# Kernel optimization log

Measured on AMD Instinct MI355X. Metric: run time of the kernel, lower is better.

Reference implementation:

```python
import jax, jax.numpy as jnp
import numpy as np
import math

B, H, S, D = 8, 16, 1024, 64


def setup_inputs() -> dict:
    key = jax.random.key(0)
    kq, kk, kv, kl = jax.random.split(key, 4)
    queries = jax.random.normal(kq, (B * H, S, D), dtype=jnp.float32)
    keys = jax.random.normal(kk, (B * H, S, D), dtype=jnp.float32)
    values = jax.random.normal(kv, (B * H, S, D), dtype=jnp.float32)
    valid_lens = jax.random.randint(kl, (B,), 0, 1024, dtype=jnp.int64)
    return {"queries": queries, "keys": keys, "values": values, "valid_lens": valid_lens}


def reference(queries, keys, values, valid_lens):
    d = queries.shape[-1]
    seq_len = queries.shape[1]
    b = valid_lens.shape[0]
    h = queries.shape[0] // b
    scale = 1.0 / math.sqrt(d)
    # [BH, S, S] scores, faithful to bmm(q, k^T)/sqrt(d)
    scores = jnp.einsum("bqd,bkd->bqk", queries, keys) * scale
    # encode_mask: mask[b, q, k] = (k >= valid_lens[b]) for 1-D valid_lens
    key_mask = jnp.arange(seq_len) >= valid_lens[:, None]  # [B, S]
    scores = scores.reshape(b, h, seq_len, seq_len)
    # masked_fill with 1e-6 (NOT -inf), faithful to the original
    scores = jnp.where(key_mask[:, None, None, :], jnp.float32(1e-6), scores)
    attn = jax.nn.softmax(scores, axis=-1)
    out = jnp.einsum("bhqk,bhkd->bhqd", attn, values.reshape(b, h, seq_len, d))
    return out.reshape(b * h, seq_len, d)
```

## Files before the change

### kernel.cpp

```cpp
#include <hip/hip_runtime.h>
#include <hip/hip_bf16.h>

typedef short short4v __attribute__((ext_vector_type(4)));
typedef short short8v __attribute__((ext_vector_type(8)));
typedef float floatx4 __attribute__((ext_vector_type(4)));

#define SLEN 1024
#define DDIM 64
#define NBH  128
#define PSTR 72

__device__ __forceinline__ unsigned short f2bf(float f) {
  union { float f; unsigned int u; } v; v.f = f;
  unsigned int u = v.u;
  u += 0x7fffu + ((u >> 16) & 1u);
  return (unsigned short)(u >> 16);
}

__device__ __forceinline__ unsigned int pkbf(float a, float b) {
  __hip_bfloat162 h = __float22bfloat162_rn(float2{a, b});
  union { __hip_bfloat162 h; unsigned int u; } c; c.h = h;
  return c.u;
}

__device__ __forceinline__ void ld_lds16(const void* g, void* l) {
  __builtin_amdgcn_global_load_lds(
      (const __attribute__((address_space(1))) void*)g,
      (__attribute__((address_space(3))) void*)l, 16, 0, 0);
}

__global__ __launch_bounds__(256)
void prep_k(const float* __restrict__ Kg, unsigned short* __restrict__ wsK) {
  const int t = blockIdx.x * 256 + threadIdx.x;
  const int tile = t >> 9;
  const int q = t & 511;
  const int r = q >> 3, gr = q & 7;
  const float4 f0 = *(const float4*)(Kg + (size_t)t * 8);
  const float4 f1 = *(const float4*)(Kg + (size_t)t * 8 + 4);
  short8v s;
  s[0]=(short)f2bf(f0.x); s[1]=(short)f2bf(f0.y); s[2]=(short)f2bf(f0.z); s[3]=(short)f2bf(f0.w);
  s[4]=(short)f2bf(f1.x); s[5]=(short)f2bf(f1.y); s[6]=(short)f2bf(f1.z); s[7]=(short)f2bf(f1.w);
  *(short8v*)(wsK + (size_t)tile * 4096 + r * 64 + ((gr ^ (r & 7)) * 8)) = s;
}

__global__ __launch_bounds__(256)
void prep_v(const float* __restrict__ Vg, unsigned short* __restrict__ wsVT,
            float* __restrict__ CS) {
  const int w = threadIdx.x >> 6;
  const int d = threadIdx.x & 63;
  const int tile = blockIdx.x * 4 + w;
  const int bh = tile >> 4, ch = tile & 15;
  const float* src = Vg + ((size_t)(bh * SLEN + ch * 64) * DDIM) + d;
  unsigned short* dst = wsVT + (size_t)tile * 4096 + d * 64;
  float sum = 0.f;
  #pragma unroll
  for (int gg = 0; gg < 8; ++gg) {
    short8v s;
    #pragma unroll
    for (int j = 0; j < 8; ++j) {
      const float x = src[(size_t)(gg * 8 + j) * DDIM];
      sum += x;
      s[j] = (short)f2bf(x);
    }
    *(short8v*)(dst + ((gg ^ (d & 7)) * 8)) = s;
  }
  if (CS) CS[(size_t)tile * 64 + d] = sum;
}

__global__ __launch_bounds__(64)
void prep_sv(float* __restrict__ CS) {
  const int bh = blockIdx.x;
  const int d  = threadIdx.x;
  float acc = 0.f;
  for (int ch = 15; ch >= 0; --ch) {
    const size_t idx = ((size_t)bh * 16 + ch) * 64 + d;
    acc += CS[idx];
    CS[idx] = acc;
  }
}

__global__ __launch_bounds__(256)
void attn_main(const float* __restrict__ Qg, const unsigned short* __restrict__ wsK,
               const unsigned short* __restrict__ wsVT, const float* __restrict__ SV,
               const int* __restrict__ vraw, float* __restrict__ Og)
{
  __shared__ unsigned short K_lds[2][4096];
  __shared__ unsigned short VT_lds[2][4096];
  __shared__ unsigned short P_lds[4][32 * PSTR];

  const int t  = threadIdx.x;
  const int w  = t >> 6;
  const int ln = t & 15;
  const int g  = (t >> 4) & 3;
  const int q0 = blockIdx.x * 128;
  const int bh = blockIdx.y;

  int vl;
  {
    const bool is64 = (vraw[1] == 0) && (vraw[3] == 0) && (vraw[5] == 0) && (vraw[7] == 0);
    const int b = bh >> 4;
    vl = is64 ? vraw[2 * b] : vraw[b];
  }
  const int full_ch     = vl >> 6;
  const int has_partial = (vl & 63) ? 1 : 0;
  const int nch         = SV ? (full_ch + has_partial) : 16;
  const int tail_start  = full_ch + has_partial;

  const float qs = 0.125f * 1.44269504f;
  short8v bq[2][2];
  #pragma unroll
  for (int nt = 0; nt < 2; ++nt) {
    const float* qp = Qg + ((size_t)bh * SLEN + q0 + w * 32 + nt * 16 + ln) * DDIM;
    #pragma unroll
    for (int st = 0; st < 2; ++st) {
      const float4 f0 = *(const float4*)(qp + st * 32 + g * 8);
      const float4 f1 = *(const float4*)(qp + st * 32 + g * 8 + 4);
      short8v a;
      a[0]=(short)f2bf(f0.x*qs); a[1]=(short)f2bf(f0.y*qs);
      a[2]=(short)f2bf(f0.z*qs); a[3]=(short)f2bf(f0.w*qs);
      a[4]=(short)f2bf(f1.x*qs); a[5]=(short)f2bf(f1.y*qs);
      a[6]=(short)f2bf(f1.z*qs); a[7]=(short)f2bf(f1.w*qs);
      bq[nt][st] = a;
    }
  }

  const int l7  = ln & 7;
  const int sw0 = ((g) ^ l7) * 8;
  const int sw1 = ((4 + g) ^ l7) * 8;

  short8v ones;
  #pragma unroll
  for (int j = 0; j < 8; ++j) ones[j] = (short)0x3F80;

  floatx4 o[2][4], lacc[2];
  #pragma unroll
  for (int m = 0; m < 2; ++m) {
    lacc[m] = (floatx4){0.f, 0.f, 0.f, 0.f};
    #pragma unroll
    for (int f = 0; f < 4; ++f) o[m][f] = (floatx4){0.f, 0.f, 0.f, 0.f};
  }

  const size_t tbase = (size_t)bh * 16 * 4096;
  auto issue = [&](int ch, int b) {
    const unsigned short* gk = wsK  + tbase + (size_t)ch * 4096;
    const unsigned short* gv = wsVT + tbase + (size_t)ch * 4096;
    ld_lds16(gk + (size_t)t * 8,         &K_lds[b][t * 8]);
    ld_lds16(gk + (size_t)(t + 256) * 8, &K_lds[b][(t + 256) * 8]);
    ld_lds16(gv + (size_t)t * 8,         &VT_lds[b][t * 8]);
    ld_lds16(gv + (size_t)(t + 256) * 8, &VT_lds[b][(t + 256) * 8]);
  };

  if (nch > 0) issue(0, 0);

  for (int ch = 0; ch < nch; ++ch) {
    const int b = ch & 1;
    if (ch + 1 < nch) {
      issue(ch + 1, b ^ 1);
      __builtin_amdgcn_s_waitcnt(0x0f74);
    } else {
      __builtin_amdgcn_s_waitcnt(0x0f70);
    }
    __builtin_amdgcn_s_barrier();

    floatx4 c[4][2];
    #pragma unroll
    for (int mt = 0; mt < 4; ++mt) {
      const short8v a0 = *(const short8v*)&K_lds[b][(mt * 16 + ln) * 64 + sw0];
      const short8v a1 = *(const short8v*)&K_lds[b][(mt * 16 + ln) * 64 + sw1];
      #pragma unroll
      for (int nt = 0; nt < 2; ++nt) {
        floatx4 acc = (floatx4){0.f, 0.f, 0.f, 0.f};
        acc = __builtin_amdgcn_mfma_f32_16x16x32_bf16(a0, bq[nt][0], acc, 0, 0, 0);
        acc = __builtin_amdgcn_mfma_f32_16x16x32_bf16(a1, bq[nt][1], acc, 0, 0, 0);
        c[mt][nt] = acc;
      }
    }

    const bool fullv = (ch < full_ch);
    #pragma unroll
    for (int mt = 0; mt < 4; ++mt) {
      const int kg = ch * 64 + mt * 16 + g * 4;
      #pragma unroll
      for (int nt = 0; nt < 2; ++nt) {
        float p[4];
        if (fullv) {
          #pragma unroll
          for (int i = 0; i < 4; ++i) p[i] = __builtin_amdgcn_exp2f(c[mt][nt][i]);
        } else {
          #pragma unroll
          for (int i = 0; i < 4; ++i) {
            const float x = (kg + i < vl) ? c[mt][nt][i] : 0.0f;
            p[i] = __builtin_amdgcn_exp2f(x);
          }
        }
        union { short4v v; unsigned int u[2]; } pk;
        pk.u[0] = pkbf(p[0], p[1]);
        pk.u[1] = pkbf(p[2], p[3]);
        *(short4v*)&P_lds[w][(nt * 16 + ln) * PSTR + mt * 16 + g * 4] = pk.v;
      }
    }

    #pragma unroll
    for (int st = 0; st < 2; ++st) {
      const short8v ap0 = *(const short8v*)&P_lds[w][(ln)      * PSTR + st * 32 + g * 8];
      const short8v ap1 = *(const short8v*)&P_lds[w][(16 + ln) * PSTR + st * 32 + g * 8];
      lacc[0] = __builtin_amdgcn_mfma_f32_16x16x32_bf16(ap0, ones, lacc[0], 0, 0, 0);
      lacc[1] = __builtin_amdgcn_mfma_f32_16x16x32_bf16(ap1, ones, lacc[1], 0, 0, 0);
      const int sw = (st == 0) ? sw0 : sw1;
      #pragma unroll
      for (int f = 0; f < 4; ++f) {
        const short8v bv = *(const short8v*)&VT_lds[b][(f * 16 + ln) * 64 + sw];
        o[0][f] = __builtin_amdgcn_mfma_f32_16x16x32_bf16(ap0, bv, o[0][f], 0, 0, 0);
        o[1][f] = __builtin_amdgcn_mfma_f32_16x16x32_bf16(ap1, bv, o[1][f], 0, 0, 0);
      }
    }

    if (ch + 1 < nch) __builtin_amdgcn_s_barrier();
  }

  if (SV != nullptr && tail_start < 16) {
    const float* sv = SV + ((size_t)bh * 16 + tail_start) * 64;
    float svf[4];
    #pragma unroll
    for (int f = 0; f < 4; ++f) svf[f] = sv[f * 16 + ln];
    const float ml = (float)(SLEN - tail_start * 64);
    #pragma unroll
    for (int m = 0; m < 2; ++m) {
      #pragma unroll
      for (int i = 0; i < 4; ++i) lacc[m][i] += ml;
      #pragma unroll
      for (int f = 0; f < 4; ++f)
        #pragma unroll
        for (int i = 0; i < 4; ++i) o[m][f][i] += svf[f];
    }
  }

  #pragma unroll
  for (int m = 0; m < 2; ++m) {
    #pragma unroll
    for (int i = 0; i < 4; ++i) {
      const float inv = 1.0f / lacc[m][i];
      const size_t row = (size_t)bh * SLEN + q0 + w * 32 + m * 16 + g * 4 + i;
      #pragma unroll
      for (int f = 0; f < 4; ++f)
        Og[row * DDIM + f * 16 + ln] = o[m][f][i] * inv;
    }
  }
}

#define KSTR 72
__device__ __forceinline__ float bf2f(unsigned short h) {
  union { unsigned int u; float f; } v; v.u = ((unsigned int)h) << 16;
  return v.f;
}
__global__ __launch_bounds__(256)
void attn_fwd_fallback(const float* __restrict__ Qg, const float* __restrict__ Kg,
                       const float* __restrict__ Vg, const int* __restrict__ vraw,
                       float* __restrict__ Og)
{
  __shared__ unsigned short K_lds[64 * KSTR];
  __shared__ unsigned short VT_lds[64 * KSTR];
  __shared__ unsigned short P_lds[4][32 * KSTR];
  const int t  = threadIdx.x;
  const int w  = t >> 6;
  const int ln = t & 15;
  const int g  = (t >> 4) & 3;
  const int q0 = blockIdx.x * 128;
  const int bh = blockIdx.y;
  int vl;
  {
    const bool is64 = (vraw[1] == 0) && (vraw[3] == 0) && (vraw[5] == 0) && (vraw[7] == 0);
    const int b = bh >> 4;
    vl = is64 ? vraw[2 * b] : vraw[b];
  }
  short8v aq[2][2];
  #pragma unroll
  for (int m = 0; m < 2; ++m) {
    const float* qp = Qg + ((size_t)bh * SLEN + q0 + w * 32 + m * 16 + ln) * DDIM;
    #pragma unroll
    for (int st = 0; st < 2; ++st) {
      const int d0 = st * 32 + g * 8;
      const float4 f0 = *(const float4*)(qp + d0);
      const float4 f1 = *(const float4*)(qp + d0 + 4);
      short8v a;
      a[0]=(short)f2bf(f0.x); a[1]=(short)f2bf(f0.y); a[2]=(short)f2bf(f0.z); a[3]=(short)f2bf(f0.w);
      a[4]=(short)f2bf(f1.x); a[5]=(short)f2bf(f1.y); a[6]=(short)f2bf(f1.z); a[7]=(short)f2bf(f1.w);
      aq[m][st] = a;
    }
  }
  float mrow[2][4], lrow[2][4];
  floatx4 o[2][4];
  #pragma unroll
  for (int m = 0; m < 2; ++m) {
    #pragma unroll
    for (int i = 0; i < 4; ++i) { mrow[m][i] = -INFINITY; lrow[m][i] = 0.f; }
    #pragma unroll
    for (int f = 0; f < 4; ++f) o[m][f] = (floatx4){0.f, 0.f, 0.f, 0.f};
  }
  const float scale = 0.125f;
  for (int ch = 0; ch < SLEN / 64; ++ch) {
    const int k0 = ch * 64;
    __syncthreads();
    {
      const int c4 = (t & 15) * 4;
      const int r0 = t >> 4;
      const float* kp = Kg + ((size_t)bh * SLEN + k0 + r0) * DDIM + c4;
      #pragma unroll
      for (int r = 0; r < 4; ++r) {
        const float4 v = *(const float4*)(kp + (size_t)(16 * r) * DDIM);
        short4v bq2;
        bq2[0]=(short)f2bf(v.x); bq2[1]=(short)f2bf(v.y); bq2[2]=(short)f2bf(v.z); bq2[3]=(short)f2bf(v.w);
        *(short4v*)&K_lds[(r0 + 16 * r) * KSTR + c4] = bq2;
      }
    }
    {
      const int kb = (t >> 4) * 4;
      const int db = (t & 15) * 4;
      const float* vp = Vg + ((size_t)bh * SLEN + k0 + kb) * DDIM + db;
      const float4 r0 = *(const float4*)(vp);
      const float4 r1 = *(const float4*)(vp + DDIM);
      const float4 r2 = *(const float4*)(vp + 2 * DDIM);
      const float4 r3 = *(const float4*)(vp + 3 * DDIM);
      short4v wa, wb, wc, wd;
      wa[0]=(short)f2bf(r0.x); wa[1]=(short)f2bf(r1.x); wa[2]=(short)f2bf(r2.x); wa[3]=(short)f2bf(r3.x);
      wb[0]=(short)f2bf(r0.y); wb[1]=(short)f2bf(r1.y); wb[2]=(short)f2bf(r2.y); wb[3]=(short)f2bf(r3.y);
      wc[0]=(short)f2bf(r0.z); wc[1]=(short)f2bf(r1.z); wc[2]=(short)f2bf(r2.z); wc[3]=(short)f2bf(r3.z);
      wd[0]=(short)f2bf(r0.w); wd[1]=(short)f2bf(r1.w); wd[2]=(short)f2bf(r2.w); wd[3]=(short)f2bf(r3.w);
      *(short4v*)&VT_lds[(db + 0) * KSTR + kb] = wa;
      *(short4v*)&VT_lds[(db + 1) * KSTR + kb] = wb;
      *(short4v*)&VT_lds[(db + 2) * KSTR + kb] = wc;
      *(short4v*)&VT_lds[(db + 3) * KSTR + kb] = wd;
    }
    __syncthreads();
    floatx4 c[2][4];
    #pragma unroll
    for (int m = 0; m < 2; ++m)
      #pragma unroll
      for (int f = 0; f < 4; ++f) c[m][f] = (floatx4){0.f, 0.f, 0.f, 0.f};
    #pragma unroll
    for (int f = 0; f < 4; ++f) {
      const short8v b0 = *(const short8v*)&K_lds[(16 * f + ln) * KSTR + g * 8];
      const short8v b1 = *(const short8v*)&K_lds[(16 * f + ln) * KSTR + 32 + g * 8];
      #pragma unroll
      for (int m = 0; m < 2; ++m) {
        c[m][f] = __builtin_amdgcn_mfma_f32_16x16x32_bf16(aq[m][0], b0, c[m][f], 0, 0, 0);
        c[m][f] = __builtin_amdgcn_mfma_f32_16x16x32_bf16(aq[m][1], b1, c[m][f], 0, 0, 0);
      }
    }
    #pragma unroll
    for (int m = 0; m < 2; ++m) {
      float s[4][4];
      #pragma unroll
      for (int f = 0; f < 4; ++f) {
        const int kgl = k0 + 16 * f + ln;
        const bool valid = kgl < vl;
        #pragma unroll
        for (int i = 0; i < 4; ++i)
          s[f][i] = valid ? c[m][f][i] * scale : 1e-6f;
      }
      #pragma unroll
      for (int i = 0; i < 4; ++i) {
        float r = fmaxf(fmaxf(s[0][i], s[1][i]), fmaxf(s[2][i], s[3][i]));
        r = fmaxf(r, __shfl_xor(r, 1));
        r = fmaxf(r, __shfl_xor(r, 2));
        r = fmaxf(r, __shfl_xor(r, 4));
        r = fmaxf(r, __shfl_xor(r, 8));
        const float mn = fmaxf(mrow[m][i], r);
        const float al = __expf(mrow[m][i] - mn);
        mrow[m][i] = mn;
        float rs = 0.f;
        #pragma unroll
        for (int f = 0; f < 4; ++f) {
          const unsigned short pb = f2bf(__expf(s[f][i] - mn));
          P_lds[w][(m * 16 + g * 4 + i) * KSTR + 16 * f + ln] = pb;
          rs += bf2f(pb);
        }
        rs += __shfl_xor(rs, 1);
        rs += __shfl_xor(rs, 2);
        rs += __shfl_xor(rs, 4);
        rs += __shfl_xor(rs, 8);
        lrow[m][i] = lrow[m][i] * al + rs;
        #pragma unroll
        for (int f = 0; f < 4; ++f) o[m][f][i] *= al;
      }
    }
    #pragma unroll
    for (int st = 0; st < 2; ++st) {
      const short8v ap0 = *(const short8v*)&P_lds[w][(ln)*KSTR + st * 32 + g * 8];
      const short8v ap1 = *(const short8v*)&P_lds[w][(16 + ln) * KSTR + st * 32 + g * 8];
      #pragma unroll
      for (int f = 0; f < 4; ++f) {
        const short8v bv = *(const short8v*)&VT_lds[(16 * f + ln) * KSTR + st * 32 + g * 8];
        o[0][f] = __builtin_amdgcn_mfma_f32_16x16x32_bf16(ap0, bv, o[0][f], 0, 0, 0);
        o[1][f] = __builtin_amdgcn_mfma_f32_16x16x32_bf16(ap1, bv, o[1][f], 0, 0, 0);
      }
    }
  }
  #pragma unroll
  for (int m = 0; m < 2; ++m) {
    float inv[4];
    #pragma unroll
    for (int i = 0; i < 4; ++i) inv[i] = 1.0f / lrow[m][i];
    #pragma unroll
    for (int f = 0; f < 4; ++f) {
      #pragma unroll
      for (int i = 0; i < 4; ++i) {
        const size_t row = (size_t)bh * SLEN + q0 + w * 32 + m * 16 + g * 4 + i;
        Og[row * DDIM + 16 * f + ln] = o[m][f][i] * inv[i];
      }
    }
  }
}

extern "C" void kernel_launch(void* const* d_in, const int* in_sizes, int n_in,
                              void* d_out, int out_size, void* d_ws, size_t ws_size,
                              hipStream_t stream) {
  const float* Q = (const float*)d_in[0];
  const float* K = (const float*)d_in[1];
  const float* V = (const float*)d_in[2];
  const int*  vl = (const int*)d_in[3];
  float* out = (float*)d_out;

  const size_t ws_kv = (size_t)2 * NBH * SLEN * DDIM * 2;
  const size_t ws_sv = ws_kv + (size_t)NBH * 16 * 64 * 4;

  if (ws_size >= ws_kv) {
    unsigned short* wsK  = (unsigned short*)d_ws;
    unsigned short* wsVT = wsK + (size_t)NBH * SLEN * DDIM;
    float* CS = (ws_size >= ws_sv) ? (float*)((char*)d_ws + ws_kv) : nullptr;
    prep_k<<<4096, 256, 0, stream>>>(K, wsK);
    prep_v<<<512, 256, 0, stream>>>(V, wsVT, CS);
    if (CS) prep_sv<<<NBH, 64, 0, stream>>>(CS);
    attn_main<<<dim3(SLEN / 128, NBH), dim3(256), 0, stream>>>(Q, wsK, wsVT, CS, vl, out);
  } else {
    attn_fwd_fallback<<<dim3(SLEN / 128, NBH), dim3(256), 0, stream>>>(Q, K, V, vl, out);
  }
}
```

Measured before the change: 174.9 us.

## Load K/V fragments directly from global, merge prep kernels, drop LDS staging

Measured after the change: 214.2 us. 1.22x slower.

```diff
diff --git a/kernel.cpp b/kernel.cpp
--- a/kernel.cpp
+++ b/kernel.cpp
@@ -23,69 +23,47 @@
   return c.u;
 }
 
-__device__ __forceinline__ void ld_lds16(const void* g, void* l) {
-  __builtin_amdgcn_global_load_lds(
-      (const __attribute__((address_space(1))) void*)g,
-      (__attribute__((address_space(3))) void*)l, 16, 0, 0);
-}
-
 __global__ __launch_bounds__(256)
-void prep_k(const float* __restrict__ Kg, unsigned short* __restrict__ wsK) {
-  const int t = blockIdx.x * 256 + threadIdx.x;
-  const int tile = t >> 9;
-  const int q = t & 511;
-  const int r = q >> 3, gr = q & 7;
-  const float4 f0 = *(const float4*)(Kg + (size_t)t * 8);
-  const float4 f1 = *(const float4*)(Kg + (size_t)t * 8 + 4);
-  short8v s;
-  s[0]=(short)f2bf(f0.x); s[1]=(short)f2bf(f0.y); s[2]=(short)f2bf(f0.z); s[3]=(short)f2bf(f0.w);
-  s[4]=(short)f2bf(f1.x); s[5]=(short)f2bf(f1.y); s[6]=(short)f2bf(f1.z); s[7]=(short)f2bf(f1.w);
-  *(short8v*)(wsK + (size_t)tile * 4096 + r * 64 + ((gr ^ (r & 7)) * 8)) = s;
-}
-
-__global__ __launch_bounds__(256)
-void prep_v(const float* __restrict__ Vg, unsigned short* __restrict__ wsVT,
-            float* __restrict__ CS) {
-  const int w = threadIdx.x >> 6;
-  const int d = threadIdx.x & 63;
-  const int tile = blockIdx.x * 4 + w;
-  const int bh = tile >> 4, ch = tile & 15;
-  const float* src = Vg + ((size_t)(bh * SLEN + ch * 64) * DDIM) + d;
-  unsigned short* dst = wsVT + (size_t)tile * 4096 + d * 64;
-  float sum = 0.f;
-  #pragma unroll
-  for (int gg = 0; gg < 8; ++gg) {
+void prep_kv(const float* __restrict__ Kg, const float* __restrict__ Vg,
+             unsigned short* __restrict__ wsK, unsigned short* __restrict__ wsVT,
+             float* __restrict__ CS) {
+  const int bx = blockIdx.x;
+  if (bx < 4096) {
+    const int t = bx * 256 + threadIdx.x;
+    const float4 f0 = *(const float4*)(Kg + (size_t)t * 8);
+    const float4 f1 = *(const float4*)(Kg + (size_t)t * 8 + 4);
     short8v s;
-    #pragma unroll
-    for (int j = 0; j < 8; ++j) {
-      const float x = src[(size_t)(gg * 8 + j) * DDIM];
-      sum += x;
-      s[j] = (short)f2bf(x);
-    }
-    *(short8v*)(dst + ((gg ^ (d & 7)) * 8)) = s;
-  }
-  if (CS) CS[(size_t)tile * 64 + d] = sum;
-}
-
-__global__ __launch_bounds__(64)
-void prep_sv(float* __restrict__ CS) {
-  const int bh = blockIdx.x;
-  const int d  = threadIdx.x;
-  float acc = 0.f;
-  for (int ch = 15; ch >= 0; --ch) {
-    const size_t idx = ((size_t)bh * 16 + ch) * 64 + d;
-    acc += CS[idx];
-    CS[idx] = acc;
+    s[0]=(short)f2bf(f0.x); s[1]=(short)f2bf(f0.y); s[2]=(short)f2bf(f0.z); s[3]=(short)f2bf(f0.w);
+    s[4]=(short)f2bf(f1.x); s[5]=(short)f2bf(f1.y); s[6]=(short)f2bf(f1.z); s[7]=(short)f2bf(f1.w);
+    *(short8v*)(wsK + (size_t)t * 8) = s;
+  } else {
+    const int w = threadIdx.x >> 6;
+    const int d = threadIdx.x & 63;
+    const int tile = (bx - 4096) * 4 + w;
+    const int bh = tile >> 4, ch = tile & 15;
+    const float* src = Vg + ((size_t)(bh * SLEN + ch * 64) * DDIM) + d;
+    unsigned short* dst = wsVT + (size_t)tile * 4096 + d * 64;
+    float sum = 0.f;
+    #pragma unroll
+    for (int gg = 0; gg < 8; ++gg) {
+      short8v s;
+      #pragma unroll
+      for (int j = 0; j < 8; ++j) {
+        const float x = src[(size_t)(gg * 8 + j) * DDIM];
+        sum += x;
+        s[j] = (short)f2bf(x);
+      }
+      *(short8v*)(dst + gg * 8) = s;
+    }
+    if (CS) CS[(size_t)tile * 64 + d] = sum;
   }
 }
 
 __global__ __launch_bounds__(256)
 void attn_main(const float* __restrict__ Qg, const unsigned short* __restrict__ wsK,
-               const unsigned short* __restrict__ wsVT, const float* __restrict__ SV,
+               const unsigned short* __restrict__ wsVT, const float* __restrict__ CS,
                const int* __restrict__ vraw, float* __restrict__ Og)
 {
-  __shared__ unsigned short K_lds[2][4096];
-  __shared__ unsigned short VT_lds[2][4096];
   __shared__ unsigned short P_lds[4][32 * PSTR];
 
   const int t  = threadIdx.x;
@@ -103,7 +81,7 @@
   }
   const int full_ch     = vl >> 6;
   const int has_partial = (vl & 63) ? 1 : 0;
-  const int nch         = SV ? (full_ch + has_partial) : 16;
+  const int nch         = CS ? (full_ch + has_partial) : 16;
   const int tail_start  = full_ch + has_partial;
 
   const float qs = 0.125f * 1.44269504f;
@@ -124,10 +102,6 @@
     }
   }
 
-  const int l7  = ln & 7;
-  const int sw0 = ((g) ^ l7) * 8;
-  const int sw1 = ((4 + g) ^ l7) * 8;
-
   short8v ones;
   #pragma unroll
   for (int j = 0; j < 8; ++j) ones[j] = (short)0x3F80;
@@ -140,41 +114,40 @@
     for (int f = 0; f < 4; ++f) o[m][f] = (floatx4){0.f, 0.f, 0.f, 0.f};
   }
 
-  const size_t tbase = (size_t)bh * 16 * 4096;
-  auto issue = [&](int ch, int b) {
-    const unsigned short* gk = wsK  + tbase + (size_t)ch * 4096;
-    const unsigned short* gv = wsVT + tbase + (size_t)ch * 4096;
-    ld_lds16(gk + (size_t)t * 8,         &K_lds[b][t * 8]);
-    ld_lds16(gk + (size_t)(t + 256) * 8, &K_lds[b][(t + 256) * 8]);
-    ld_lds16(gv + (size_t)t * 8,         &VT_lds[b][t * 8]);
-    ld_lds16(gv + (size_t)(t + 256) * 8, &VT_lds[b][(t + 256) * 8]);
-  };
-
-  if (nch > 0) issue(0, 0);
+  const unsigned short* gk0 = wsK  + (size_t)bh * 16 * 4096;
+  const unsigned short* gv0 = wsVT + (size_t)bh * 16 * 4096;
 
   for (int ch = 0; ch < nch; ++ch) {
-    const int b = ch & 1;
-    if (ch + 1 < nch) {
-      issue(ch + 1, b ^ 1);
-      __builtin_amdgcn_s_waitcnt(0x0f74);
-    } else {
-      __builtin_amdgcn_s_waitcnt(0x0f70);
-    }
-    __builtin_amdgcn_s_barrier();
+    const unsigned short* gk = gk0 + (size_t)ch * 4096;
+    const unsigned short* gv = gv0 + (size_t)ch * 4096;
+
+    short8v ak0[4], ak1[4];
+    #pragma unroll
+    for (int mt = 0; mt < 4; ++mt) {
+      ak0[mt] = *(const short8v*)(gk + (mt * 16 + ln) * 64 + g * 8);
+      ak1[mt] = *(const short8v*)(gk + (mt * 16 + ln) * 64 + 32 + g * 8);
+    }
 
     floatx4 c[4][2];
+    __builtin_amdgcn_s_setprio(1);
     #pragma unroll
     for (int mt = 0; mt < 4; ++mt) {
-      const short8v a0 = *(const short8v*)&K_lds[b][(mt * 16 + ln) * 64 + sw0];
-      const short8v a1 = *(const short8v*)&K_lds[b][(mt * 16 + ln) * 64 + sw1];
       #pragma unroll
       for (int nt = 0; nt < 2; ++nt) {
         floatx4 acc = (floatx4){0.f, 0.f, 0.f, 0.f};
-        acc = __builtin_amdgcn_mfma_f32_16x16x32_bf16(a0, bq[nt][0], acc, 0, 0, 0);
-        acc = __builtin_amdgcn_mfma_f32_16x16x32_bf16(a1, bq[nt][1], acc, 0, 0, 0);
+        acc = __builtin_amdgcn_mfma_f32_16x16x32_bf16(ak0[mt], bq[nt][0], acc, 0, 0, 0);
+        acc = __builtin_amdgcn_mfma_f32_16x16x32_bf16(ak1[mt], bq[nt][1], acc, 0, 0, 0);
         c[mt][nt] = acc;
       }
     }
+    __builtin_amdgcn_s_setprio(0);
+
+    short8v av[2][4];
+    #pragma unroll
+    for (int st = 0; st < 2; ++st)
+      #pragma unroll
+      for (int f = 0; f < 4; ++f)
+        av[st][f] = *(const short8v*)(gv + (f * 16 + ln) * 64 + st * 32 + g * 8);
 
     const bool fullv = (ch < full_ch);
     #pragma unroll
@@ -204,25 +177,25 @@
     for (int st = 0; st < 2; ++st) {
       const short8v ap0 = *(const short8v*)&P_lds[w][(ln)      * PSTR + st * 32 + g * 8];
       const short8v ap1 = *(const short8v*)&P_lds[w][(16 + ln) * PSTR + st * 32 + g * 8];
+      __builtin_amdgcn_s_setprio(1);
       lacc[0] = __builtin_amdgcn_mfma_f32_16x16x32_bf16(ap0, ones, lacc[0], 0, 0, 0);
       lacc[1] = __builtin_amdgcn_mfma_f32_16x16x32_bf16(ap1, ones, lacc[1], 0, 0, 0);
-      const int sw = (st == 0) ? sw0 : sw1;
       #pragma unroll
       for (int f = 0; f < 4; ++f) {
-        const short8v bv = *(const short8v*)&VT_lds[b][(f * 16 + ln) * 64 + sw];
-        o[0][f] = __builtin_amdgcn_mfma_f32_16x16x32_bf16(ap0, bv, o[0][f], 0, 0, 0);
-        o[1][f] = __builtin_amdgcn_mfma_f32_16x16x32_bf16(ap1, bv, o[1][f], 0, 0, 0);
-      }
-    }
-
-    if (ch + 1 < nch) __builtin_amdgcn_s_barrier();
-  }
-
-  if (SV != nullptr && tail_start < 16) {
-    const float* sv = SV + ((size_t)bh * 16 + tail_start) * 64;
-    float svf[4];
-    #pragma unroll
-    for (int f = 0; f < 4; ++f) svf[f] = sv[f * 16 + ln];
+        o[0][f] = __builtin_amdgcn_mfma_f32_16x16x32_bf16(ap0, av[st][f], o[0][f], 0, 0, 0);
+        o[1][f] = __builtin_amdgcn_mfma_f32_16x16x32_bf16(ap1, av[st][f], o[1][f], 0, 0, 0);
+      }
+      __builtin_amdgcn_s_setprio(0);
+    }
+  }
+
+  if (CS != nullptr && tail_start < 16) {
+    float svf[4] = {0.f, 0.f, 0.f, 0.f};
+    for (int ch = tail_start; ch < 16; ++ch) {
+      const float* cs = CS + ((size_t)bh * 16 + ch) * 64;
+      #pragma unroll
+      for (int f = 0; f < 4; ++f) svf[f] += cs[f * 16 + ln];
+    }
     const float ml = (float)(SLEN - tail_start * 64);
     #pragma unroll
     for (int m = 0; m < 2; ++m) {
@@ -428,9 +401,7 @@
     unsigned short* wsK  = (unsigned short*)d_ws;
     unsigned short* wsVT = wsK + (size_t)NBH * SLEN * DDIM;
     float* CS = (ws_size >= ws_sv) ? (float*)((char*)d_ws + ws_kv) : nullptr;
-    prep_k<<<4096, 256, 0, stream>>>(K, wsK);
-    prep_v<<<512, 256, 0, stream>>>(V, wsVT, CS);
-    if (CS) prep_sv<<<NBH, 64, 0, stream>>>(CS);
+    prep_kv<<<4608, 256, 0, stream>>>(K, V, wsK, wsVT, CS);
     attn_main<<<dim3(SLEN / 128, NBH), dim3(256), 0, stream>>>(Q, wsK, wsVT, CS, vl, out);
   } else {
     attn_fwd_fallback<<<dim3(SLEN / 128, NBH), dim3(256), 0, stream>>>(Q, K, V, vl, out);
```

## Fuse prep kernels, keep P in registers via permlane swaps, transpose PV MFMA

Applied to the files above, without the earlier changes.

Measured after the change: 194.7 us. 11.4% more time.

```diff
diff --git a/kernel.cpp b/kernel.cpp
--- a/kernel.cpp
+++ b/kernel.cpp
@@ -4,11 +4,11 @@
 typedef short short4v __attribute__((ext_vector_type(4)));
 typedef short short8v __attribute__((ext_vector_type(8)));
 typedef float floatx4 __attribute__((ext_vector_type(4)));
+typedef unsigned int uint2v __attribute__((ext_vector_type(2)));
 
 #define SLEN 1024
 #define DDIM 64
 #define NBH  128
-#define PSTR 72
 
 __device__ __forceinline__ unsigned short f2bf(float f) {
   union { float f; unsigned int u; } v; v.f = f;
@@ -23,6 +23,23 @@
   return c.u;
 }
 
+__device__ __forceinline__ void pl32sw(unsigned int &a, unsigned int &b) {
+#if __has_builtin(__builtin_amdgcn_permlane32_swap)
+  uint2v r = __builtin_amdgcn_permlane32_swap(a, b, false, false);
+  a = r[0]; b = r[1];
+#else
+  asm volatile("s_nop 1\n\tv_permlane32_swap_b32 %0, %1" : "+v"(a), "+v"(b));
+#endif
+}
+__device__ __forceinline__ void pl16sw(unsigned int &a, unsigned int &b) {
+#if __has_builtin(__builtin_amdgcn_permlane16_swap)
+  uint2v r = __builtin_amdgcn_permlane16_swap(a, b, false, false);
+  a = r[0]; b = r[1];
+#else
+  asm volatile("s_nop 1\n\tv_permlane16_swap_b32 %0, %1" : "+v"(a), "+v"(b));
+#endif
+}
+
 __device__ __forceinline__ void ld_lds16(const void* g, void* l) {
   __builtin_amdgcn_global_load_lds(
       (const __attribute__((address_space(1))) void*)g,
@@ -30,66 +47,54 @@
 }
 
 __global__ __launch_bounds__(256)
-void prep_k(const float* __restrict__ Kg, unsigned short* __restrict__ wsK) {
-  const int t = blockIdx.x * 256 + threadIdx.x;
-  const int tile = t >> 9;
-  const int q = t & 511;
-  const int r = q >> 3, gr = q & 7;
-  const float4 f0 = *(const float4*)(Kg + (size_t)t * 8);
-  const float4 f1 = *(const float4*)(Kg + (size_t)t * 8 + 4);
-  short8v s;
-  s[0]=(short)f2bf(f0.x); s[1]=(short)f2bf(f0.y); s[2]=(short)f2bf(f0.z); s[3]=(short)f2bf(f0.w);
-  s[4]=(short)f2bf(f1.x); s[5]=(short)f2bf(f1.y); s[6]=(short)f2bf(f1.z); s[7]=(short)f2bf(f1.w);
-  *(short8v*)(wsK + (size_t)tile * 4096 + r * 64 + ((gr ^ (r & 7)) * 8)) = s;
-}
-
-__global__ __launch_bounds__(256)
-void prep_v(const float* __restrict__ Vg, unsigned short* __restrict__ wsVT,
-            float* __restrict__ CS) {
-  const int w = threadIdx.x >> 6;
-  const int d = threadIdx.x & 63;
-  const int tile = blockIdx.x * 4 + w;
-  const int bh = tile >> 4, ch = tile & 15;
-  const float* src = Vg + ((size_t)(bh * SLEN + ch * 64) * DDIM) + d;
-  unsigned short* dst = wsVT + (size_t)tile * 4096 + d * 64;
-  float sum = 0.f;
-  #pragma unroll
-  for (int gg = 0; gg < 8; ++gg) {
+void prep_kv(const float* __restrict__ Kg, const float* __restrict__ Vg,
+             unsigned short* __restrict__ wsK, unsigned short* __restrict__ wsVT,
+             float* __restrict__ CS) {
+  const int bx = blockIdx.x;
+  if (bx < 4096) {
+    const int t = bx * 256 + threadIdx.x;
+    const int tile = t >> 9;
+    const int q = t & 511;
+    const int r = q >> 3, gr = q & 7;
+    const float4 f0 = *(const float4*)(Kg + (size_t)t * 8);
+    const float4 f1 = *(const float4*)(Kg + (size_t)t * 8 + 4);
     short8v s;
-    #pragma unroll
-    for (int j = 0; j < 8; ++j) {
-      const float x = src[(size_t)(gg * 8 + j) * DDIM];
-      sum += x;
-      s[j] = (short)f2bf(x);
-    }
-    *(short8v*)(dst + ((gg ^ (d & 7)) * 8)) = s;
-  }
-  if (CS) CS[(size_t)tile * 64 + d] = sum;
-}
-
-__global__ __launch_bounds__(64)
-void prep_sv(float* __restrict__ CS) {
-  const int bh = blockIdx.x;
-  const int d  = threadIdx.x;
-  float acc = 0.f;
-  for (int ch = 15; ch >= 0; --ch) {
-    const size_t idx = ((size_t)bh * 16 + ch) * 64 + d;
-    acc += CS[idx];
-    CS[idx] = acc;
+    s[0]=(short)f2bf(f0.x); s[1]=(short)f2bf(f0.y); s[2]=(short)f2bf(f0.z); s[3]=(short)f2bf(f0.w);
+    s[4]=(short)f2bf(f1.x); s[5]=(short)f2bf(f1.y); s[6]=(short)f2bf(f1.z); s[7]=(short)f2bf(f1.w);
+    *(short8v*)(wsK + (size_t)tile * 4096 + r * 64 + ((gr ^ (r & 7)) * 8)) = s;
+  } else {
+    const int w = threadIdx.x >> 6;
+    const int d = threadIdx.x & 63;
+    const int tile = (bx - 4096) * 4 + w;
+    const int bh = tile >> 4, ch = tile & 15;
+    const float* src = Vg + ((size_t)(bh * SLEN + ch * 64) * DDIM) + d;
+    unsigned short* dst = wsVT + (size_t)tile * 4096 + d * 64;
+    float sum = 0.f;
+    #pragma unroll
+    for (int gg = 0; gg < 8; ++gg) {
+      short8v s;
+      #pragma unroll
+      for (int j = 0; j < 8; ++j) {
+        const float x = src[(size_t)(gg * 8 + j) * DDIM];
+        sum += x;
+        s[j] = (short)f2bf(x);
+      }
+      *(short8v*)(dst + ((gg ^ (d & 7)) * 8)) = s;
+    }
+    if (CS) CS[(size_t)tile * 64 + d] = sum;
   }
 }
 
 __global__ __launch_bounds__(256)
 void attn_main(const float* __restrict__ Qg, const unsigned short* __restrict__ wsK,
-               const unsigned short* __restrict__ wsVT, const float* __restrict__ SV,
+               const unsigned short* __restrict__ wsVT, const float* __restrict__ CS,
                const int* __restrict__ vraw, float* __restrict__ Og)
 {
   __shared__ unsigned short K_lds[2][4096];
   __shared__ unsigned short VT_lds[2][4096];
-  __shared__ unsigned short P_lds[4][32 * PSTR];
 
   const int t  = threadIdx.x;
-  const int w  = t >> 6;
+  const int ww = t >> 6;
   const int ln = t & 15;
   const int g  = (t >> 4) & 3;
   const int q0 = blockIdx.x * 128;
@@ -103,14 +108,14 @@
   }
   const int full_ch     = vl >> 6;
   const int has_partial = (vl & 63) ? 1 : 0;
-  const int nch         = SV ? (full_ch + has_partial) : 16;
+  const int nch         = CS ? (full_ch + has_partial) : 16;
   const int tail_start  = full_ch + has_partial;
 
   const float qs = 0.125f * 1.44269504f;
   short8v bq[2][2];
   #pragma unroll
   for (int nt = 0; nt < 2; ++nt) {
-    const float* qp = Qg + ((size_t)bh * SLEN + q0 + w * 32 + nt * 16 + ln) * DDIM;
+    const float* qp = Qg + ((size_t)bh * SLEN + q0 + ww * 32 + nt * 16 + ln) * DDIM;
     #pragma unroll
     for (int st = 0; st < 2; ++st) {
       const float4 f0 = *(const float4*)(qp + st * 32 + g * 8);
@@ -132,12 +137,12 @@
   #pragma unroll
   for (int j = 0; j < 8; ++j) ones[j] = (short)0x3F80;
 
-  floatx4 o[2][4], lacc[2];
+  floatx4 ot[2][4], lacc[2];
   #pragma unroll
   for (int m = 0; m < 2; ++m) {
     lacc[m] = (floatx4){0.f, 0.f, 0.f, 0.f};
     #pragma unroll
-    for (int f = 0; f < 4; ++f) o[m][f] = (floatx4){0.f, 0.f, 0.f, 0.f};
+    for (int f = 0; f < 4; ++f) ot[m][f] = (floatx4){0.f, 0.f, 0.f, 0.f};
   }
 
   const size_t tbase = (size_t)bh * 16 * 4096;
@@ -176,6 +181,7 @@
       }
     }
 
+    unsigned int pk0[4][2], pk1[4][2];
     const bool fullv = (ch < full_ch);
     #pragma unroll
     for (int mt = 0; mt < 4; ++mt) {
@@ -193,57 +199,76 @@
             p[i] = __builtin_amdgcn_exp2f(x);
           }
         }
-        union { short4v v; unsigned int u[2]; } pk;
-        pk.u[0] = pkbf(p[0], p[1]);
-        pk.u[1] = pkbf(p[2], p[3]);
-        *(short4v*)&P_lds[w][(nt * 16 + ln) * PSTR + mt * 16 + g * 4] = pk.v;
-      }
-    }
-
+        pk0[mt][nt] = pkbf(p[0], p[1]);
+        pk1[mt][nt] = pkbf(p[2], p[3]);
+      }
+    }
+
+    short8v bp[2][2];
     #pragma unroll
     for (int st = 0; st < 2; ++st) {
-      const short8v ap0 = *(const short8v*)&P_lds[w][(ln)      * PSTR + st * 32 + g * 8];
-      const short8v ap1 = *(const short8v*)&P_lds[w][(16 + ln) * PSTR + st * 32 + g * 8];
-      lacc[0] = __builtin_amdgcn_mfma_f32_16x16x32_bf16(ap0, ones, lacc[0], 0, 0, 0);
-      lacc[1] = __builtin_amdgcn_mfma_f32_16x16x32_bf16(ap1, ones, lacc[1], 0, 0, 0);
+      #pragma unroll
+      for (int nt = 0; nt < 2; ++nt) {
+        unsigned int a0 = pk0[2 * st][nt], b0 = pk0[2 * st + 1][nt];
+        unsigned int a1 = pk1[2 * st][nt], b1 = pk1[2 * st + 1][nt];
+        pl32sw(a0, b0); pl16sw(a0, b0);
+        pl32sw(a1, b1); pl16sw(a1, b1);
+        union { short8v s; unsigned int u[4]; } bb;
+        bb.u[0] = a0; bb.u[1] = a1; bb.u[2] = b0; bb.u[3] = b1;
+        bp[st][nt] = bb.s;
+      }
+    }
+
+    #pragma unroll
+    for (int st = 0; st < 2; ++st) {
+      lacc[0] = __builtin_amdgcn_mfma_f32_16x16x32_bf16(ones, bp[st][0], lacc[0], 0, 0, 0);
+      lacc[1] = __builtin_amdgcn_mfma_f32_16x16x32_bf16(ones, bp[st][1], lacc[1], 0, 0, 0);
       const int sw = (st == 0) ? sw0 : sw1;
       #pragma unroll
       for (int f = 0; f < 4; ++f) {
-        const short8v bv = *(const short8v*)&VT_lds[b][(f * 16 + ln) * 64 + sw];
-        o[0][f] = __builtin_amdgcn_mfma_f32_16x16x32_bf16(ap0, bv, o[0][f], 0, 0, 0);
-        o[1][f] = __builtin_amdgcn_mfma_f32_16x16x32_bf16(ap1, bv, o[1][f], 0, 0, 0);
+        const short8v av = *(const short8v*)&VT_lds[b][(f * 16 + ln) * 64 + sw];
+        ot[0][f] = __builtin_amdgcn_mfma_f32_16x16x32_bf16(av, bp[st][0], ot[0][f], 0, 0, 0);
+        ot[1][f] = __builtin_amdgcn_mfma_f32_16x16x32_bf16(av, bp[st][1], ot[1][f], 0, 0, 0);
       }
     }
 
     if (ch + 1 < nch) __builtin_amdgcn_s_barrier();
   }
 
-  if (SV != nullptr && tail_start < 16) {
-    const float* sv = SV + ((size_t)bh * 16 + tail_start) * 64;
-    float svf[4];
-    #pragma unroll
-    for (int f = 0; f < 4; ++f) svf[f] = sv[f * 16 + ln];
+  if (CS != nullptr && tail_start < 16) {
+    floatx4 sv4[4];
+    #pragma unroll
+    for (int f = 0; f < 4; ++f) sv4[f] = (floatx4){0.f, 0.f, 0.f, 0.f};
+    for (int ch2 = tail_start; ch2 < 16; ++ch2) {
+      const float* cs = CS + ((size_t)bh * 16 + ch2) * 64 + g * 4;
+      #pragma unroll
+      for (int f = 0; f < 4; ++f) {
+        const float4 v4 = *(const float4*)(cs + f * 16);
+        sv4[f][0] += v4.x; sv4[f][1] += v4.y; sv4[f][2] += v4.z; sv4[f][3] += v4.w;
+      }
+    }
     const float ml = (float)(SLEN - tail_start * 64);
     #pragma unroll
-    for (int m = 0; m < 2; ++m) {
-      #pragma unroll
-      for (int i = 0; i < 4; ++i) lacc[m][i] += ml;
+    for (int nt = 0; nt < 2; ++nt) {
+      #pragma unroll
+      for (int i = 0; i < 4; ++i) lacc[nt][i] += ml;
       #pragma unroll
       for (int f = 0; f < 4; ++f)
         #pragma unroll
-        for (int i = 0; i < 4; ++i) o[m][f][i] += svf[f];
-    }
-  }
-
-  #pragma unroll
-  for (int m = 0; m < 2; ++m) {
-    #pragma unroll
-    for (int i = 0; i < 4; ++i) {
-      const float inv = 1.0f / lacc[m][i];
-      const size_t row = (size_t)bh * SLEN + q0 + w * 32 + m * 16 + g * 4 + i;
-      #pragma unroll
-      for (int f = 0; f < 4; ++f)
-        Og[row * DDIM + f * 16 + ln] = o[m][f][i] * inv;
+        for (int i = 0; i < 4; ++i) ot[nt][f][i] += sv4[f][i];
+    }
+  }
+
+  #pragma unroll
+  for (int nt = 0; nt < 2; ++nt) {
+    const float inv = 1.0f / lacc[nt][0];
+    float* orow = Og + ((size_t)bh * SLEN + q0 + ww * 32 + nt * 16 + ln) * DDIM + g * 4;
+    #pragma unroll
+    for (int f = 0; f < 4; ++f) {
+      float4 v4;
+      v4.x = ot[nt][f][0] * inv; v4.y = ot[nt][f][1] * inv;
+      v4.z = ot[nt][f][2] * inv; v4.w = ot[nt][f][3] * inv;
+      *(float4*)(orow + f * 16) = v4;
     }
   }
 }
@@ -428,9 +453,7 @@
     unsigned short* wsK  = (unsigned short*)d_ws;
     unsigned short* wsVT = wsK + (size_t)NBH * SLEN * DDIM;
     float* CS = (ws_size >= ws_sv) ? (float*)((char*)d_ws + ws_kv) : nullptr;
-    prep_k<<<4096, 256, 0, stream>>>(K, wsK);
-    prep_v<<<512, 256, 0, stream>>>(V, wsVT, CS);
-    if (CS) prep_sv<<<NBH, 64, 0, stream>>>(CS);
+    prep_kv<<<4608, 256, 0, stream>>>(K, V, wsK, wsVT, CS);
     attn_main<<<dim3(SLEN / 128, NBH), dim3(256), 0, stream>>>(Q, wsK, wsVT, CS, vl, out);
   } else {
     attn_fwd_fallback<<<dim3(SLEN / 128, NBH), dim3(256), 0, stream>>>(Q, K, V, vl, out);
```

## Fuse K/V prep, skip masked chunks, sort blocks by work across XCDs

Applied to the files above, without the earlier changes.

Result: no change. 178.2 us (+1.9%).

```diff
diff --git a/kernel.cpp b/kernel.cpp
--- a/kernel.cpp
+++ b/kernel.cpp
@@ -29,60 +29,100 @@
       (__attribute__((address_space(3))) void*)l, 16, 0, 0);
 }
 
+__device__ __forceinline__ int decode_vl(const int* __restrict__ vraw, int bh_or_b) {
+  const bool is64 = (vraw[1] == 0) && (vraw[3] == 0) && (vraw[5] == 0) && (vraw[7] == 0);
+  const int b = (bh_or_b >= 16) ? (bh_or_b >> 4) : (bh_or_b >> 4);
+  return is64 ? vraw[2 * b] : vraw[b];
+}
+
 __global__ __launch_bounds__(256)
-void prep_k(const float* __restrict__ Kg, unsigned short* __restrict__ wsK) {
-  const int t = blockIdx.x * 256 + threadIdx.x;
-  const int tile = t >> 9;
-  const int q = t & 511;
-  const int r = q >> 3, gr = q & 7;
-  const float4 f0 = *(const float4*)(Kg + (size_t)t * 8);
-  const float4 f1 = *(const float4*)(Kg + (size_t)t * 8 + 4);
-  short8v s;
-  s[0]=(short)f2bf(f0.x); s[1]=(short)f2bf(f0.y); s[2]=(short)f2bf(f0.z); s[3]=(short)f2bf(f0.w);
-  s[4]=(short)f2bf(f1.x); s[5]=(short)f2bf(f1.y); s[6]=(short)f2bf(f1.z); s[7]=(short)f2bf(f1.w);
-  *(short8v*)(wsK + (size_t)tile * 4096 + r * 64 + ((gr ^ (r & 7)) * 8)) = s;
-}
-
-__global__ __launch_bounds__(256)
-void prep_v(const float* __restrict__ Vg, unsigned short* __restrict__ wsVT,
-            float* __restrict__ CS) {
-  const int w = threadIdx.x >> 6;
-  const int d = threadIdx.x & 63;
-  const int tile = blockIdx.x * 4 + w;
-  const int bh = tile >> 4, ch = tile & 15;
-  const float* src = Vg + ((size_t)(bh * SLEN + ch * 64) * DDIM) + d;
-  unsigned short* dst = wsVT + (size_t)tile * 4096 + d * 64;
-  float sum = 0.f;
-  #pragma unroll
-  for (int gg = 0; gg < 8; ++gg) {
+void prep_kv(const float* __restrict__ Kg, const float* __restrict__ Vg,
+             unsigned short* __restrict__ wsK, unsigned short* __restrict__ wsVT,
+             float* __restrict__ CS, const int* __restrict__ vraw, int do_skip) {
+  const int bx = blockIdx.x;
+  if (bx < 4096) {
+    const int tile = bx >> 1;
+    if (do_skip) {
+      const int bh = tile >> 4, ch = tile & 15;
+      const int vl = decode_vl(vraw, bh);
+      const int nch = (vl >> 6) + ((vl & 63) ? 1 : 0);
+      if (ch >= nch) return;
+    }
+    const int t = bx * 256 + threadIdx.x;
+    const int q = t & 511;
+    const int r = q >> 3, gr = q & 7;
+    const float4 f0 = *(const float4*)(Kg + (size_t)t * 8);
+    const float4 f1 = *(const float4*)(Kg + (size_t)t * 8 + 4);
     short8v s;
-    #pragma unroll
-    for (int j = 0; j < 8; ++j) {
-      const float x = src[(size_t)(gg * 8 + j) * DDIM];
-      sum += x;
-      s[j] = (short)f2bf(x);
-    }
-    *(short8v*)(dst + ((gg ^ (d & 7)) * 8)) = s;
-  }
-  if (CS) CS[(size_t)tile * 64 + d] = sum;
+    s[0]=(short)f2bf(f0.x); s[1]=(short)f2bf(f0.y); s[2]=(short)f2bf(f0.z); s[3]=(short)f2bf(f0.w);
+    s[4]=(short)f2bf(f1.x); s[5]=(short)f2bf(f1.y); s[6]=(short)f2bf(f1.z); s[7]=(short)f2bf(f1.w);
+    *(short8v*)(wsK + (size_t)(bx >> 1) * 4096 + r * 64 + ((gr ^ (r & 7)) * 8)) = s;
+  } else {
+    const int w = threadIdx.x >> 6;
+    const int d = threadIdx.x & 63;
+    const int tile = (bx - 4096) * 4 + w;
+    const int bh = tile >> 4, ch = tile & 15;
+    bool do_store = true;
+    if (do_skip) {
+      const int vl = decode_vl(vraw, bh);
+      const int nch = (vl >> 6) + ((vl & 63) ? 1 : 0);
+      do_store = (ch < nch);
+    }
+    const float* src = Vg + ((size_t)(bh * SLEN + ch * 64) * DDIM) + d;
+    unsigned short* dst = wsVT + (size_t)tile * 4096 + d * 64;
+    float sum = 0.f;
+    #pragma unroll
+    for (int gg = 0; gg < 8; ++gg) {
+      short8v s;
+      #pragma unroll
+      for (int j = 0; j < 8; ++j) {
+        const float x = src[(size_t)(gg * 8 + j) * DDIM];
+        sum += x;
+        s[j] = (short)f2bf(x);
+      }
+      if (do_store) *(short8v*)(dst + ((gg ^ (d & 7)) * 8)) = s;
+    }
+    if (CS) CS[(size_t)tile * 64 + d] = sum;
+  }
 }
 
 __global__ __launch_bounds__(64)
-void prep_sv(float* __restrict__ CS) {
-  const int bh = blockIdx.x;
-  const int d  = threadIdx.x;
-  float acc = 0.f;
-  for (int ch = 15; ch >= 0; --ch) {
-    const size_t idx = ((size_t)bh * 16 + ch) * 64 + d;
-    acc += CS[idx];
-    CS[idx] = acc;
+void prep_sv(float* __restrict__ CS, const int* __restrict__ vraw, int* __restrict__ SRT) {
+  const int blk = blockIdx.x;
+  if (blk < NBH) {
+    const int d = threadIdx.x;
+    float acc = 0.f;
+    for (int ch = 15; ch >= 0; --ch) {
+      const size_t idx = ((size_t)blk * 16 + ch) * 64 + d;
+      acc += CS[idx];
+      CS[idx] = acc;
+    }
+  } else {
+    const int x = threadIdx.x;
+    if (x < 8) {
+      int key[16];
+      #pragma unroll
+      for (int k = 0; k < 16; ++k) {
+        const int vv = decode_vl(vraw, x + 8 * k);
+        key[k] = (vv >> 6) + ((vv & 63) ? 1 : 0);
+      }
+      #pragma unroll
+      for (int i = 0; i < 16; ++i) {
+        int rank = 0;
+        #pragma unroll
+        for (int k2 = 0; k2 < 16; ++k2)
+          rank += (int)((key[k2] > key[i]) || (key[k2] == key[i] && k2 < i));
+        SRT[x * 16 + rank] = x + 8 * i;
+      }
+    }
   }
 }
 
 __global__ __launch_bounds__(256)
 void attn_main(const float* __restrict__ Qg, const unsigned short* __restrict__ wsK,
                const unsigned short* __restrict__ wsVT, const float* __restrict__ SV,
-               const int* __restrict__ vraw, float* __restrict__ Og)
+               const int* __restrict__ SRT, const int* __restrict__ vraw,
+               float* __restrict__ Og)
 {
   __shared__ unsigned short K_lds[2][4096];
   __shared__ unsigned short VT_lds[2][4096];
@@ -92,15 +132,22 @@
   const int w  = t >> 6;
   const int ln = t & 15;
   const int g  = (t >> 4) & 3;
-  const int q0 = blockIdx.x * 128;
-  const int bh = blockIdx.y;
-
-  int vl;
-  {
-    const bool is64 = (vraw[1] == 0) && (vraw[3] == 0) && (vraw[5] == 0) && (vraw[7] == 0);
-    const int b = bh >> 4;
-    vl = is64 ? vraw[2 * b] : vraw[b];
-  }
+
+  int bh, q0;
+  if (SRT) {
+    const int xcd  = blockIdx.x & 7;
+    const int lidx = blockIdx.x >> 3;
+    const int cu   = lidx & 31;
+    const int j    = lidx >> 5;
+    const int r    = j * 32 + ((j & 1) ? (31 - cu) : cu);
+    bh = SRT[xcd * 16 + (r >> 3)];
+    q0 = (r & 7) * 128;
+  } else {
+    bh = blockIdx.x & 127;
+    q0 = (blockIdx.x >> 7) * 128;
+  }
+
+  const int vl          = decode_vl(vraw, bh);
   const int full_ch     = vl >> 6;
   const int has_partial = (vl & 63) ? 1 : 0;
   const int nch         = SV ? (full_ch + has_partial) : 16;
@@ -163,6 +210,7 @@
     __builtin_amdgcn_s_barrier();
 
     floatx4 c[4][2];
+    __builtin_amdgcn_s_setprio(1);
     #pragma unroll
     for (int mt = 0; mt < 4; ++mt) {
       const short8v a0 = *(const short8v*)&K_lds[b][(mt * 16 + ln) * 64 + sw0];
@@ -175,6 +223,7 @@
         c[mt][nt] = acc;
       }
     }
+    __builtin_amdgcn_s_setprio(0);
 
     const bool fullv = (ch < full_ch);
     #pragma unroll
@@ -204,6 +253,7 @@
     for (int st = 0; st < 2; ++st) {
       const short8v ap0 = *(const short8v*)&P_lds[w][(ln)      * PSTR + st * 32 + g * 8];
       const short8v ap1 = *(const short8v*)&P_lds[w][(16 + ln) * PSTR + st * 32 + g * 8];
+      __builtin_amdgcn_s_setprio(1);
       lacc[0] = __builtin_amdgcn_mfma_f32_16x16x32_bf16(ap0, ones, lacc[0], 0, 0, 0);
       lacc[1] = __builtin_amdgcn_mfma_f32_16x16x32_bf16(ap1, ones, lacc[1], 0, 0, 0);
       const int sw = (st == 0) ? sw0 : sw1;
@@ -213,6 +263,7 @@
         o[0][f] = __builtin_amdgcn_mfma_f32_16x16x32_bf16(ap0, bv, o[0][f], 0, 0, 0);
         o[1][f] = __builtin_amdgcn_mfma_f32_16x16x32_bf16(ap1, bv, o[1][f], 0, 0, 0);
       }
+      __builtin_amdgcn_s_setprio(0);
     }
 
     if (ch + 1 < nch) __builtin_amdgcn_s_barrier();
@@ -421,17 +472,18 @@
   const int*  vl = (const int*)d_in[3];
   float* out = (float*)d_out;
 
-  const size_t ws_kv = (size_t)2 * NBH * SLEN * DDIM * 2;
-  const size_t ws_sv = ws_kv + (size_t)NBH * 16 * 64 * 4;
+  const size_t ws_kv  = (size_t)2 * NBH * SLEN * DDIM * 2;
+  const size_t ws_cs  = ws_kv + (size_t)NBH * 16 * 64 * 4;
+  const size_t ws_all = ws_cs + 8 * 16 * 4;
 
   if (ws_size >= ws_kv) {
     unsigned short* wsK  = (unsigned short*)d_ws;
     unsigned short* wsVT = wsK + (size_t)NBH * SLEN * DDIM;
-    float* CS = (ws_size >= ws_sv) ? (float*)((char*)d_ws + ws_kv) : nullptr;
-    prep_k<<<4096, 256, 0, stream>>>(K, wsK);
-    prep_v<<<512, 256, 0, stream>>>(V, wsVT, CS);
-    if (CS) prep_sv<<<NBH, 64, 0, stream>>>(CS);
-    attn_main<<<dim3(SLEN / 128, NBH), dim3(256), 0, stream>>>(Q, wsK, wsVT, CS, vl, out);
+    float* CS = (ws_size >= ws_all) ? (float*)((char*)d_ws + ws_kv) : nullptr;
+    int*  SRT = CS ? (int*)((char*)d_ws + ws_cs) : nullptr;
+    prep_kv<<<4608, 256, 0, stream>>>(K, V, wsK, wsVT, CS, vl, CS ? 1 : 0);
+    if (CS) prep_sv<<<NBH + 1, 64, 0, stream>>>(CS, vl, SRT);
+    attn_main<<<dim3(1024), dim3(256), 0, stream>>>(Q, wsK, wsVT, CS, SRT, vl, out);
   } else {
     attn_fwd_fallback<<<dim3(SLEN / 128, NBH), dim3(256), 0, stream>>>(Q, K, V, vl, out);
   }
```
